# Optimization experiments

Measured on AMD Instinct MI355X. Metric: run time of the kernel, lower is better.

## Reference

```python
import jax, jax.numpy as jnp
import numpy as np

# Module hyperparameters (from init_kwargs)
N_HEAD = 16
D_K = 64
D_V = 64
TEMPERATURE = 0.7
TOP_K = 32
NEG_MIN = jnp.finfo(jnp.float32).min


def setup_inputs() -> dict:
    key = jax.random.key(0)
    ks = jax.random.split(key, 7)
    B, L, E = 2, 2048, 1024
    return {
        "q": jax.random.normal(ks[0], (B, L, E), jnp.float32),
        "k": jax.random.normal(ks[1], (B, L, E), jnp.float32),
        "v": jax.random.normal(ks[2], (B, L, D_V), jnp.float32),
        "w_q": jax.random.normal(ks[3], (N_HEAD * D_K, E), jnp.float32) * (E ** -0.5),
        "w_k": jax.random.normal(ks[4], (N_HEAD * D_K, E), jnp.float32) * (E ** -0.5),
        "w_v": jax.random.normal(ks[5], (N_HEAD * D_V, D_V), jnp.float32) * (D_V ** -0.5),
        "w_fc": jax.random.normal(ks[6], (D_V, N_HEAD * D_V), jnp.float32) * ((N_HEAD * D_V) ** -0.5),
    }


def _topk_restrict(logits):
    # Keep exactly TOP_K entries per row (scatter of top-k indices), fill rest with dtype min.
    B, H, Lq, Lk = logits.shape
    _, idx = jax.lax.top_k(logits, TOP_K)  # [B,H,Lq,TOP_K]
    bb = jnp.arange(B)[:, None, None, None]
    hh = jnp.arange(H)[None, :, None, None]
    qq = jnp.arange(Lq)[None, None, :, None]
    keep = jnp.zeros(logits.shape, bool).at[bb, hh, qq, idx].set(True)
    return jnp.where(keep, logits, NEG_MIN)


def reference(q, k, v, w_q, w_k, w_v, w_fc):
    B, Lq, _ = q.shape
    Lk = k.shape[1]
    Lv = v.shape[1]
    # Projections (bias-free linears), split heads: [B, H, L, d]
    q_proj = (q @ w_q.T).reshape(B, Lq, N_HEAD, D_K).transpose(0, 2, 1, 3)
    k_proj = (k @ w_k.T).reshape(B, Lk, N_HEAD, D_K).transpose(0, 2, 1, 3)
    v_proj = (v @ w_v.T).reshape(B, Lv, N_HEAD, D_V).transpose(0, 2, 1, 3)
    # Scaled QK^T in float32, then temperature scaling.
    logits = jnp.einsum("bhqd,bhkd->bhqk", q_proj / (D_K ** 0.5), k_proj).astype(jnp.float32)
    logits = logits / TEMPERATURE
    # Top-k restriction of attention logits (query_mask_flat=None -> applied to all queries).
    logits = _topk_restrict(logits)
    # Softmax selection; dropout is identity in eval / p=0.
    attn_probs = jax.nn.softmax(logits, axis=-1).astype(v.dtype)
    mixed = jnp.einsum("bhqk,bhkd->bhqd", attn_probs, v_proj)
    out = mixed.transpose(0, 2, 1, 3).reshape(B, Lq, N_HEAD * D_V)
    output = out @ w_fc.T
    return output, attn_probs
```

## Files before the change

### kernel.cpp

```cpp
#include <hip/hip_runtime.h>
#include <stdint.h>
#include <float.h>

constexpr int L = 2048;
constexpr int H = 16;
constexpr float SCALE = 0.17857142857142858f;
constexpr int OUT0 = 2 * 2048 * 64;
constexpr float QSTEP = 0.0625f;

typedef float f32x4 __attribute__((ext_vector_type(4)));
typedef short s16x8 __attribute__((ext_vector_type(8)));
typedef unsigned short u16x8 __attribute__((ext_vector_type(8)));

__device__ __forceinline__ float wave_fmax(float x) {
#pragma unroll
  for (int s = 32; s; s >>= 1) x = fmaxf(x, __shfl_xor(x, s));
  return x;
}
__device__ __forceinline__ float wave_fsum(float x) {
#pragma unroll
  for (int s = 32; s; s >>= 1) x += __shfl_xor(x, s);
  return x;
}
__device__ __forceinline__ int wave_isum(int x) {
#pragma unroll
  for (int s = 32; s; s >>= 1) x += __shfl_xor(x, s);
  return x;
}
__device__ __forceinline__ unsigned f2sort(float f) {
  unsigned u = __float_as_uint(f);
  return (u & 0x80000000u) ? ~u : (u | 0x80000000u);
}
__device__ __forceinline__ void lds_fence() {
  __asm__ __volatile__("s_waitcnt lgkmcnt(0)" ::: "memory");
}
__device__ __forceinline__ unsigned short rne_bf16(float f) {
  unsigned u = __float_as_uint(f);
  return (unsigned short)((u + 0x7fffu + ((u >> 16) & 1u)) >> 16);
}

template <int K, bool EMIT>
__global__ __launch_bounds__(256) void proj_kernel(const float* __restrict__ X,
                                                   const float* __restrict__ W,
                                                   float* __restrict__ Y,
                                                   unsigned short* __restrict__ Yb,
                                                   float bscale) {
  __shared__ float As[16][128];
  __shared__ float Bs[16][64];
  const int t = threadIdx.x;
  const int tx = t & 15;
  const int ty = t >> 4;
  const int m0 = blockIdx.y * 128;
  const int n0 = blockIdx.x * 64;
  const int ar = t >> 1, ac = (t & 1) * 8;
  const int br = t >> 2, bc = (t & 3) * 4;
  const float* xg = X + (size_t)(m0 + ar) * K + ac;
  const float* wg = W + (size_t)(n0 + br) * K + bc;
  float acc[8][4] = {};
  for (int k0 = 0; k0 < K; k0 += 16) {
    float4 a0 = *(const float4*)(xg + k0);
    float4 a1 = *(const float4*)(xg + k0 + 4);
    float4 b0 = *(const float4*)(wg + k0);
    __syncthreads();
    As[ac + 0][ar] = a0.x; As[ac + 1][ar] = a0.y; As[ac + 2][ar] = a0.z; As[ac + 3][ar] = a0.w;
    As[ac + 4][ar] = a1.x; As[ac + 5][ar] = a1.y; As[ac + 6][ar] = a1.z; As[ac + 7][ar] = a1.w;
    Bs[bc + 0][br] = b0.x; Bs[bc + 1][br] = b0.y; Bs[bc + 2][br] = b0.z; Bs[bc + 3][br] = b0.w;
    __syncthreads();
#pragma unroll
    for (int kk = 0; kk < 16; ++kk) {
      float4 av0 = *(const float4*)&As[kk][ty * 8];
      float4 av1 = *(const float4*)&As[kk][ty * 8 + 4];
      float4 bv = *(const float4*)&Bs[kk][tx * 4];
      float ar8[8] = {av0.x, av0.y, av0.z, av0.w, av1.x, av1.y, av1.z, av1.w};
      float br4[4] = {bv.x, bv.y, bv.z, bv.w};
#pragma unroll
      for (int i = 0; i < 8; ++i)
#pragma unroll
        for (int j = 0; j < 4; ++j) acc[i][j] = fmaf(ar8[i], br4[j], acc[i][j]);
    }
  }
  const int n = n0 + tx * 4;
  const int h = n >> 6, d = n & 63;
#pragma unroll
  for (int i = 0; i < 8; ++i) {
    int mm = m0 + ty * 8 + i;
    int b = mm >> 11, l = mm & 2047;
    size_t off = (((size_t)b * H + h) * L + l) * 64 + d;
    *(float4*)&Y[off] = make_float4(acc[i][0], acc[i][1], acc[i][2], acc[i][3]);
    if (EMIT) {
      ushort4 bv4;
      bv4.x = rne_bf16(acc[i][0] * bscale);
      bv4.y = rne_bf16(acc[i][1] * bscale);
      bv4.z = rne_bf16(acc[i][2] * bscale);
      bv4.w = rne_bf16(acc[i][3] * bscale);
      *(ushort4*)&Yb[off] = bv4;
    }
  }
}

constexpr int ALD = 72;
constexpr int CTB = 136;

__global__ __launch_bounds__(256) void alogits_kernel(const unsigned short* __restrict__ Qb,
                                                      const unsigned short* __restrict__ Kb,
                                                      char* __restrict__ AL) {
  __shared__ union {
    unsigned short qk[2][128 * ALD];
    char ct[128 * CTB];
  } sh;
  const int t = threadIdx.x;
  const int bh = blockIdx.z;
  const int m0 = blockIdx.y * 128, n0 = blockIdx.x * 128;
  const unsigned short* Qg = Qb + (size_t)bh * L * 64 + (size_t)m0 * 64;
  const unsigned short* Kg = Kb + (size_t)bh * L * 64 + (size_t)n0 * 64;
#pragma unroll
  for (int i = 0; i < 4; ++i) {
    int blk = t * 4 + i;
    int r = blk >> 3, lb = blk & 7;
    *(u16x8*)&sh.qk[0][r * ALD + lb * 8] = *(const u16x8*)&Qg[r * 64 + lb * 8];
    *(u16x8*)&sh.qk[1][r * ALD + lb * 8] = *(const u16x8*)&Kg[r * 64 + lb * 8];
  }
  __syncthreads();
  const int wv = t >> 6, lane = t & 63;
  const int wm = (wv & 1) * 64, wn = (wv >> 1) * 64;
  const int fr = lane & 15, quad = lane >> 4;
  f32x4 acc[16];
#pragma unroll
  for (int i = 0; i < 16; ++i) acc[i] = (f32x4){0.f, 0.f, 0.f, 0.f};
#pragma unroll
  for (int kh = 0; kh < 2; ++kh) {
    s16x8 a[4], b[4];
#pragma unroll
    for (int mi = 0; mi < 4; ++mi)
      a[mi] = *(const s16x8*)&sh.qk[0][(wm + mi * 16 + fr) * ALD + kh * 32 + quad * 8];
#pragma unroll
    for (int ni = 0; ni < 4; ++ni)
      b[ni] = *(const s16x8*)&sh.qk[1][(wn + ni * 16 + fr) * ALD + kh * 32 + quad * 8];
#pragma unroll
    for (int mi = 0; mi < 4; ++mi)
#pragma unroll
      for (int ni = 0; ni < 4; ++ni)
        acc[mi * 4 + ni] = __builtin_amdgcn_mfma_f32_16x16x32_bf16(
            a[mi], b[ni], acc[mi * 4 + ni], 0, 0, 0);
  }
  __syncthreads();
#pragma unroll
  for (int mi = 0; mi < 4; ++mi)
#pragma unroll
    for (int ni = 0; ni < 4; ++ni) {
      int col = wn + ni * 16 + fr;
#pragma unroll
      for (int r = 0; r < 4; ++r) {
        int rowl = wm + mi * 16 + quad * 4 + r;
        float sc = acc[mi * 4 + ni][r] * 16.0f;
        sc = fminf(fmaxf(sc, -127.0f), 127.0f);
        sh.ct[rowl * CTB + col] = (char)__float2int_rn(sc);
      }
    }
  __syncthreads();
  char* Abase = AL + (size_t)bh * L * L;
  const int rq = lane >> 4;
  const int cq = (lane & 15) * 8;
#pragma unroll
  for (int it = 0; it < 8; ++it) {
    int row = wv * 32 + it * 4 + rq;
    uint2 v8 = *(const uint2*)&sh.ct[row * CTB + cq];
    __builtin_nontemporal_store(v8.x, (unsigned*)&Abase[(size_t)(m0 + row) * L + n0 + cq]);
    __builtin_nontemporal_store(v8.y, (unsigned*)&Abase[(size_t)(m0 + row) * L + n0 + cq + 4]);
  }
}

__global__ __launch_bounds__(256) void select_kernel(const char* __restrict__ AL,
                                                     const float* __restrict__ Qp,
                                                     const float* __restrict__ Kp,
                                                     const float* __restrict__ Vp,
                                                     float* __restrict__ Probs,
                                                     float* __restrict__ Mixed) {
  __shared__ float prow[4][2048];
  __shared__ float qbuf[4][64];
  __shared__ float cbuf[4][64];
  __shared__ int ibufc[4][64];
  __shared__ float pbuf[4][32];
  __shared__ int ibuf[4][32];
  const int lane = threadIdx.x & 63;
  const int w = threadIdx.x >> 6;
  const int row = blockIdx.x * 4 + w;
  const int bh = row >> 11;
  const int q = row & 2047;
  const unsigned long long below = (lane == 63) ? 0x7fffffffffffffffull
                                                : ((1ull << lane) - 1ull);
  const unsigned* Arow = (const unsigned*)(AL + (size_t)row * 2048);

  float lg[32];
#pragma unroll
  for (int u2 = 0; u2 < 8; ++u2) {
    unsigned dw = __builtin_nontemporal_load(Arow + u2 * 64 + lane);
#pragma unroll
    for (int b = 0; b < 4; ++b)
      lg[u2 * 4 + b] = (float)((char)(dw >> (8 * b))) * QSTEP;
  }
#pragma unroll
  for (int u = 0; u < 32; ++u) prow[w][u * 64 + lane] = 0.f;
  if (lane < 16)
    *(float4*)&qbuf[w][lane * 4] = *(const float4*)&Qp[((size_t)bh * L + q) * 64 + lane * 4];

  float m = lg[0];
#pragma unroll
  for (int u = 1; u < 32; ++u) m = fmaxf(m, lg[u]);
  m = wave_fmax(m);

  float T = 0.f;
  bool found = false;
  float cut = m - 2.2f;
  float lo = 0.f, hi = m;
  bool has_lo = false;
  for (int attempt = 0; attempt < 8 && !found; ++attempt) {
    int c = 0;
#pragma unroll
    for (int u = 0; u < 32; ++u) c += (lg[u] > cut) ? 1 : 0;
    c = wave_isum(c);
    if (c < 32) {
      hi = cut;
      cut = has_lo ? 0.5f * (lo + cut) : (cut - 0.45f);
    } else if (c > 64) {
      lo = cut; has_lo = true;
      cut = 0.5f * (cut + hi);
    } else {
      int base = 0;
#pragma unroll
      for (int u = 0; u < 32; ++u) {
        bool cd = lg[u] > cut;
        unsigned long long mk = __ballot(cd);
        if (cd) cbuf[w][base + __popcll(mk & below)] = lg[u];
        base += __popcll(mk);
      }
      lds_fence();
      float v2 = (lane < c) ? cbuf[w][lane] : -FLT_MAX;
#pragma unroll
      for (int size = 2; size <= 64; size <<= 1)
#pragma unroll
        for (int stride = size >> 1; stride; stride >>= 1) {
          float pv = __shfl_xor(v2, stride);
          bool lower = (lane & stride) == 0;
          bool asc = (lane & size) == 0;
          v2 = (lower == asc) ? fminf(v2, pv) : fmaxf(v2, pv);
        }
      T = __shfl(v2, 32);
      found = true;
    }
  }
  if (!found) {
    unsigned tb = 0;
    for (int bit = 31; bit >= 0; --bit) {
      unsigned cand = tb | (1u << bit);
      int c = 0;
#pragma unroll
      for (int u = 0; u < 32; ++u) c += (f2sort(lg[u]) >= cand) ? 1 : 0;
      c = wave_isum(c);
      if (c >= 32) tb = cand;
    }
    T = (tb & 0x80000000u) ? __uint_as_float(tb & 0x7fffffffu) : __uint_as_float(~tb);
  }

  float theta = T;
  int c2 = 0;
  const float margs[5] = {0.40f, 0.25f, 0.15f, 0.08f, 0.0f};
#pragma unroll
  for (int a = 0; a < 5; ++a) {
    float th = T - margs[a];
    int c = 0;
#pragma unroll
    for (int u = 0; u < 32; ++u) c += (lg[u] >= th) ? 1 : 0;
    c = wave_isum(c);
    theta = th; c2 = c;
    if (c <= 64) break;
  }
  if (c2 > 64) c2 = 64;

  {
    int base = 0;
#pragma unroll
    for (int u = 0; u < 32; ++u) {
      bool cd = lg[u] >= theta;
      unsigned long long mk = __ballot(cd);
      if (cd) {
        int s = base + __popcll(mk & below);
        if (s < 64) ibufc[w][s] = ((u >> 2) * 64 + lane) * 4 + (u & 3);
      }
      base += __popcll(mk);
    }
  }
  lds_fence();

  int myi = (lane < c2) ? ibufc[w][lane] : 0x7fffffff;
  float vex = -FLT_MAX;
  if (lane < c2) {
    const float4* K4 = (const float4*)(Kp + ((size_t)bh * L + myi) * 64);
    const float4* Q4 = (const float4*)&qbuf[w][0];
    float acc = 0.f;
#pragma unroll
    for (int dq = 0; dq < 16; ++dq) {
      float4 kv = K4[dq];
      float4 qv = Q4[dq];
      acc = fmaf(qv.x, kv.x, acc);
      acc = fmaf(qv.y, kv.y, acc);
      acc = fmaf(qv.z, kv.z, acc);
      acc = fmaf(qv.w, kv.w, acc);
    }
    vex = (acc * 0.125f) / 0.7f;
  }

  unsigned long long key = ((unsigned long long)(~f2sort(vex)) << 32) | (unsigned)myi;
#pragma unroll
  for (int size = 2; size <= 64; size <<= 1)
#pragma unroll
    for (int stride = size >> 1; stride; stride >>= 1) {
      unsigned long long pk = __shfl_xor(key, stride);
      unsigned long long mn = key < pk ? key : pk;
      unsigned long long mx = key < pk ? pk : key;
      bool keepmin = ((lane & stride) == 0) == ((lane & size) == 0);
      key = keepmin ? mn : mx;
    }
  unsigned uv = ~(unsigned)(key >> 32);
  float vs = __uint_as_float((uv & 0x80000000u) ? (uv & 0x7fffffffu) : ~uv);
  int sidx = (int)(unsigned)(key & 0xffffffffull);

  float vmax = __shfl(vs, 0);
  float e = (lane < 32) ? __expf(vs - vmax) : 0.f;
  float S = wave_fsum(e);
  float p = e / S;
  if (lane < 32) {
    pbuf[w][lane] = p;
    ibuf[w][lane] = sidx;
    prow[w][sidx] = p;
  }
  lds_fence();

  float* Prow = Probs + (size_t)row * 2048;
#pragma unroll
  for (int u = 0; u < 32; ++u)
    __builtin_nontemporal_store(prow[w][u * 64 + lane], Prow + u * 64 + lane);

  const float* Vb = Vp + (size_t)bh * L * 64;
  float accv = 0.f;
#pragma unroll
  for (int i = 0; i < 32; ++i)
    accv = fmaf(pbuf[w][i], Vb[(size_t)ibuf[w][i] * 64 + lane], accv);
  const int bb = bh >> 4, hh = bh & 15;
  Mixed[((size_t)(bb * 2048 + q)) * 1024 + hh * 64 + lane] = accv;
}

__global__ __launch_bounds__(256) void fc_kernel(const float* __restrict__ Mx,
                                                 const float* __restrict__ Wfc,
                                                 float* __restrict__ Out) {
  __shared__ float As[32][64];
  __shared__ float Ws[64][64];
  const int t = threadIdx.x;
  const int tx = t & 15;
  const int ty = t >> 4;
  const int m0 = blockIdx.x * 32;
  float acc[2][4] = {};
  for (int k0 = 0; k0 < 1024; k0 += 64) {
    __syncthreads();
    {
      int lin = t * 8;
      int rr = lin >> 6, kk = lin & 63;
      *(float4*)&As[rr][kk] = *(const float4*)&Mx[(size_t)(m0 + rr) * 1024 + k0 + kk];
      *(float4*)&As[rr][kk + 4] = *(const float4*)&Mx[(size_t)(m0 + rr) * 1024 + k0 + kk + 4];
    }
    {
      int n = t >> 2;
      int kq = (t & 3) * 16;
#pragma unroll
      for (int u = 0; u < 4; ++u) {
        float4 wv = *(const float4*)&Wfc[(size_t)n * 1024 + k0 + kq + u * 4];
        Ws[kq + u * 4 + 0][n] = wv.x;
        Ws[kq + u * 4 + 1][n] = wv.y;
        Ws[kq + u * 4 + 2][n] = wv.z;
        Ws[kq + u * 4 + 3][n] = wv.w;
      }
    }
    __syncthreads();
#pragma unroll
    for (int kk = 0; kk < 64; ++kk) {
      float a0 = As[ty][kk], a1 = As[ty + 16][kk];
      float4 wv = *(const float4*)&Ws[kk][tx * 4];
      float wr[4] = {wv.x, wv.y, wv.z, wv.w};
#pragma unroll
      for (int j = 0; j < 4; ++j) {
        acc[0][j] = fmaf(a0, wr[j], acc[0][j]);
        acc[1][j] = fmaf(a1, wr[j], acc[1][j]);
      }
    }
  }
#pragma unroll
  for (int i = 0; i < 2; ++i) {
    int mm = m0 + ty + i * 16;
    *(float4*)&Out[(size_t)mm * 64 + tx * 4] =
        make_float4(acc[i][0], acc[i][1], acc[i][2], acc[i][3]);
  }
}

extern "C" void kernel_launch(void* const* d_in, const int* in_sizes, int n_in,
                              void* d_out, int out_size, void* d_ws, size_t ws_size,
                              hipStream_t stream) {
  const float* q    = (const float*)d_in[0];
  const float* k    = (const float*)d_in[1];
  const float* v    = (const float*)d_in[2];
  const float* w_q  = (const float*)d_in[3];
  const float* w_k  = (const float*)d_in[4];
  const float* w_v  = (const float*)d_in[5];
  const float* w_fc = (const float*)d_in[6];

  float* out = (float*)d_out;
  float* probs = out + OUT0;

  float* ws = (float*)d_ws;
  float* q_proj = ws;
  float* k_proj = ws + 4194304;
  float* v_proj = ws + 8388608;
  float* mixed  = ws + 12582912;
  unsigned short* qb = (unsigned short*)(ws + 16777216);
  unsigned short* kb = (unsigned short*)(ws + 18874368);
  char* al = (char*)(ws + 20971520);

  dim3 blk(256);
  proj_kernel<1024, true><<<dim3(16, 32), blk, 0, stream>>>(q, w_q, q_proj, qb, SCALE);
  proj_kernel<1024, true><<<dim3(16, 32), blk, 0, stream>>>(k, w_k, k_proj, kb, 1.0f);
  proj_kernel<64, false><<<dim3(16, 32), blk, 0, stream>>>(v, w_v, v_proj, nullptr, 1.0f);
  alogits_kernel<<<dim3(16, 16, 32), blk, 0, stream>>>(qb, kb, al);
  select_kernel<<<dim3(16384), blk, 0, stream>>>(al, q_proj, k_proj, v_proj, probs, mixed);
  fc_kernel<<<dim3(128), blk, 0, stream>>>(mixed, w_fc, out);
}
```

Measured before the change: 1.007 ms.

## Run Q/K projections on fp16 MFMA with hi/lo split precision emulation

Replaces the scalar FP32 SIMT GEMM for the Q and K projections with a pre-split step that turns inputs and weights into fp16 high/low pairs (scaled by 256). A matrix-core GEMM then uses three fp16 MFMAs per tile to approximate FP32 accuracy, loading operands with global_load_lds into swizzled LDS. The half-precision copies for the logits kernel are now fp16 rather than bf16, with the temperature/scale folded into the int8 quantization factor. This adds a separate conversion pass with extra memory traffic and relies on the split keeping enough precision for the top-k selection.

Result: faster. 875.9 us (-13.1%).

```diff
diff --git a/kernel.cpp b/kernel.cpp
--- a/kernel.cpp
+++ b/kernel.cpp
@@ -11,6 +11,7 @@
 typedef float f32x4 __attribute__((ext_vector_type(4)));
 typedef short s16x8 __attribute__((ext_vector_type(8)));
 typedef unsigned short u16x8 __attribute__((ext_vector_type(8)));
+typedef _Float16 h16x8 __attribute__((ext_vector_type(8)));
 
 __device__ __forceinline__ float wave_fmax(float x) {
 #pragma unroll
@@ -34,9 +35,127 @@
 __device__ __forceinline__ void lds_fence() {
   __asm__ __volatile__("s_waitcnt lgkmcnt(0)" ::: "memory");
 }
-__device__ __forceinline__ unsigned short rne_bf16(float f) {
-  unsigned u = __float_as_uint(f);
-  return (unsigned short)((u + 0x7fffu + ((u >> 16) & 1u)) >> 16);
+
+__device__ __forceinline__ void gload_lds16(const void* g, void* l) {
+  __builtin_amdgcn_global_load_lds((const __attribute__((address_space(1))) void*)g,
+                                   (__attribute__((address_space(3))) void*)l, 16, 0, 0);
+}
+
+__global__ __launch_bounds__(256) void split_kernel(
+    const float* __restrict__ q, const float* __restrict__ k,
+    const float* __restrict__ wq, const float* __restrict__ wk,
+    unsigned short* __restrict__ qh, unsigned short* __restrict__ ql,
+    unsigned short* __restrict__ kh, unsigned short* __restrict__ kl,
+    unsigned short* __restrict__ wqh, unsigned short* __restrict__ wql,
+    unsigned short* __restrict__ wkh, unsigned short* __restrict__ wkl) {
+  const int y = blockIdx.y;
+  const float* src = (y == 0) ? q : (y == 1) ? k : (y == 2) ? wq : wk;
+  unsigned short* dh = (y == 0) ? qh : (y == 1) ? kh : (y == 2) ? wqh : wkh;
+  unsigned short* dl = (y == 0) ? ql : (y == 1) ? kl : (y == 2) ? wql : wkl;
+  const int n = (y < 2) ? (4096 * 1024) : (1024 * 1024);
+  int idx = (blockIdx.x * 256 + threadIdx.x) * 4;
+  const int stride = gridDim.x * 256 * 4;
+  for (; idx < n; idx += stride) {
+    float4 v = *(const float4*)(src + idx);
+    float xs[4] = {v.x, v.y, v.z, v.w};
+    unsigned short hs[4], ls[4];
+#pragma unroll
+    for (int i = 0; i < 4; ++i) {
+      float x = xs[i] * 256.0f;
+      _Float16 hh = (_Float16)x;
+      float r = x - (float)hh;
+      _Float16 ll = (_Float16)r;
+      hs[i] = __builtin_bit_cast(unsigned short, hh);
+      ls[i] = __builtin_bit_cast(unsigned short, ll);
+    }
+    *(ushort4*)(dh + idx) = make_ushort4(hs[0], hs[1], hs[2], hs[3]);
+    *(ushort4*)(dl + idx) = make_ushort4(ls[0], ls[1], ls[2], ls[3]);
+  }
+}
+
+__global__ __launch_bounds__(256) void proj_split_kernel(
+    const unsigned short* __restrict__ QH, const unsigned short* __restrict__ QL,
+    const unsigned short* __restrict__ KH, const unsigned short* __restrict__ KL,
+    const unsigned short* __restrict__ WQH, const unsigned short* __restrict__ WQL,
+    const unsigned short* __restrict__ WKH, const unsigned short* __restrict__ WKL,
+    float* __restrict__ QP, float* __restrict__ KP,
+    unsigned short* __restrict__ Q16, unsigned short* __restrict__ K16) {
+  __shared__ unsigned short sh[4][128 * 64];
+  const int t = threadIdx.x;
+  const int z = blockIdx.z;
+  const int m0 = blockIdx.y * 128;
+  const int n0 = blockIdx.x * 128;
+  const unsigned short* xh = z ? KH : QH;
+  const unsigned short* xl = z ? KL : QL;
+  const unsigned short* wh = z ? WKH : WQH;
+  const unsigned short* wl = z ? WKL : WQL;
+  float* Y = z ? KP : QP;
+  unsigned short* Y16 = z ? K16 : Q16;
+  const unsigned short* mats[4] = {xh + (size_t)m0 * 1024, xl + (size_t)m0 * 1024,
+                                   wh + (size_t)n0 * 1024, wl + (size_t)n0 * 1024};
+  const int wv = t >> 6, lane = t & 63;
+  const int wm = (wv & 1) * 64, wn = (wv >> 1) * 64;
+  const int fr = lane & 15, quad = lane >> 4;
+  f32x4 acc[16];
+#pragma unroll
+  for (int i = 0; i < 16; ++i) acc[i] = (f32x4){0.f, 0.f, 0.f, 0.f};
+
+  for (int c = 0; c < 16; ++c) {
+    const int k0 = c * 64;
+#pragma unroll
+    for (int j = 0; j < 16; ++j) {
+      const int mat = j >> 2;
+      const int idx = (j & 3) * 256 + t;
+      const int r = idx >> 3, p = idx & 7;
+      const int sb = p ^ (r & 7);
+      gload_lds16(mats[mat] + (size_t)r * 1024 + k0 + sb * 8, &sh[mat][idx * 8]);
+    }
+    __syncthreads();
+#pragma unroll
+    for (int kh2 = 0; kh2 < 2; ++kh2) {
+      h16x8 ah[4], alv[4], bh[4], blv[4];
+#pragma unroll
+      for (int mi = 0; mi < 4; ++mi) {
+        int row = wm + mi * 16 + fr;
+        int pp = (kh2 * 4 + quad) ^ (row & 7);
+        ah[mi]  = *(const h16x8*)&sh[0][row * 64 + pp * 8];
+        alv[mi] = *(const h16x8*)&sh[1][row * 64 + pp * 8];
+      }
+#pragma unroll
+      for (int ni = 0; ni < 4; ++ni) {
+        int row = wn + ni * 16 + fr;
+        int pp = (kh2 * 4 + quad) ^ (row & 7);
+        bh[ni]  = *(const h16x8*)&sh[2][row * 64 + pp * 8];
+        blv[ni] = *(const h16x8*)&sh[3][row * 64 + pp * 8];
+      }
+#pragma unroll
+      for (int mi = 0; mi < 4; ++mi)
+#pragma unroll
+        for (int ni = 0; ni < 4; ++ni) {
+          acc[mi * 4 + ni] = __builtin_amdgcn_mfma_f32_16x16x32_f16(ah[mi], bh[ni], acc[mi * 4 + ni], 0, 0, 0);
+          acc[mi * 4 + ni] = __builtin_amdgcn_mfma_f32_16x16x32_f16(ah[mi], blv[ni], acc[mi * 4 + ni], 0, 0, 0);
+          acc[mi * 4 + ni] = __builtin_amdgcn_mfma_f32_16x16x32_f16(alv[mi], bh[ni], acc[mi * 4 + ni], 0, 0, 0);
+        }
+    }
+    __syncthreads();
+  }
+#pragma unroll
+  for (int mi = 0; mi < 4; ++mi)
+#pragma unroll
+    for (int ni = 0; ni < 4; ++ni) {
+      int col = n0 + wn + ni * 16 + fr;
+      int h = col >> 6, d = col & 63;
+#pragma unroll
+      for (int r = 0; r < 4; ++r) {
+        int m = m0 + wm + mi * 16 + quad * 4 + r;
+        int b = m >> 11, l = m & 2047;
+        size_t off = (((size_t)b * H + h) * L + l) * 64 + d;
+        float val = acc[mi * 4 + ni][r] * (1.0f / 65536.0f);
+        Y[off] = val;
+        _Float16 hf = (_Float16)val;
+        Y16[off] = __builtin_bit_cast(unsigned short, hf);
+      }
+    }
 }
 
 template <int K, bool EMIT>
@@ -87,14 +206,6 @@
     int b = mm >> 11, l = mm & 2047;
     size_t off = (((size_t)b * H + h) * L + l) * 64 + d;
     *(float4*)&Y[off] = make_float4(acc[i][0], acc[i][1], acc[i][2], acc[i][3]);
-    if (EMIT) {
-      ushort4 bv4;
-      bv4.x = rne_bf16(acc[i][0] * bscale);
-      bv4.y = rne_bf16(acc[i][1] * bscale);
-      bv4.z = rne_bf16(acc[i][2] * bscale);
-      bv4.w = rne_bf16(acc[i][3] * bscale);
-      *(ushort4*)&Yb[off] = bv4;
-    }
   }
 }
 
@@ -129,18 +240,18 @@
   for (int i = 0; i < 16; ++i) acc[i] = (f32x4){0.f, 0.f, 0.f, 0.f};
 #pragma unroll
   for (int kh = 0; kh < 2; ++kh) {
-    s16x8 a[4], b[4];
+    h16x8 a[4], b[4];
 #pragma unroll
     for (int mi = 0; mi < 4; ++mi)
-      a[mi] = *(const s16x8*)&sh.qk[0][(wm + mi * 16 + fr) * ALD + kh * 32 + quad * 8];
+      a[mi] = *(const h16x8*)&sh.qk[0][(wm + mi * 16 + fr) * ALD + kh * 32 + quad * 8];
 #pragma unroll
     for (int ni = 0; ni < 4; ++ni)
-      b[ni] = *(const s16x8*)&sh.qk[1][(wn + ni * 16 + fr) * ALD + kh * 32 + quad * 8];
+      b[ni] = *(const h16x8*)&sh.qk[1][(wn + ni * 16 + fr) * ALD + kh * 32 + quad * 8];
 #pragma unroll
     for (int mi = 0; mi < 4; ++mi)
 #pragma unroll
       for (int ni = 0; ni < 4; ++ni)
-        acc[mi * 4 + ni] = __builtin_amdgcn_mfma_f32_16x16x32_bf16(
+        acc[mi * 4 + ni] = __builtin_amdgcn_mfma_f32_16x16x32_f16(
             a[mi], b[ni], acc[mi * 4 + ni], 0, 0, 0);
   }
   __syncthreads();
@@ -152,7 +263,7 @@
 #pragma unroll
       for (int r = 0; r < 4; ++r) {
         int rowl = wm + mi * 16 + quad * 4 + r;
-        float sc = acc[mi * 4 + ni][r] * 16.0f;
+        float sc = acc[mi * 4 + ni][r] * 2.8571428571428572f;
         sc = fminf(fmaxf(sc, -127.0f), 127.0f);
         sh.ct[rowl * CTB + col] = (char)__float2int_rn(sc);
       }
@@ -424,9 +535,21 @@
   unsigned short* kb = (unsigned short*)(ws + 18874368);
   char* al = (char*)(ws + 20971520);
 
+  unsigned short* qh  = (unsigned short*)((char*)d_ws + 234881024);
+  unsigned short* ql  = qh + 4194304;
+  unsigned short* kh  = ql + 4194304;
+  unsigned short* kl  = kh + 4194304;
+  unsigned short* wqh = kl + 4194304;
+  unsigned short* wql = wqh + 1048576;
+  unsigned short* wkh = wql + 1048576;
+  unsigned short* wkl = wkh + 1048576;
+
   dim3 blk(256);
-  proj_kernel<1024, true><<<dim3(16, 32), blk, 0, stream>>>(q, w_q, q_proj, qb, SCALE);
-  proj_kernel<1024, true><<<dim3(16, 32), blk, 0, stream>>>(k, w_k, k_proj, kb, 1.0f);
+  split_kernel<<<dim3(1024, 4), blk, 0, stream>>>(q, k, w_q, w_k,
+                                                  qh, ql, kh, kl, wqh, wql, wkh, wkl);
+  proj_split_kernel<<<dim3(8, 32, 2), blk, 0, stream>>>(qh, ql, kh, kl,
+                                                        wqh, wql, wkh, wkl,
+                                                        q_proj, k_proj, qb, kb);
   proj_kernel<64, false><<<dim3(16, 32), blk, 0, stream>>>(v, w_v, v_proj, nullptr, 1.0f);
   alogits_kernel<<<dim3(16, 16, 32), blk, 0, stream>>>(qb, kb, al);
   select_kernel<<<dim3(16384), blk, 0, stream>>>(al, q_proj, k_proj, v_proj, probs, mixed);
```
